# Optimization experiments

Hardware: AMD Instinct MI355X
Metric: run time of the kernel (lower is better)

Reference implementation:

```python
import jax, jax.numpy as jnp
import numpy as np

N_NODES, N_EDGES, N_GRAPHS = 8192, 32768, 256
FXD, HEADS = 78, 10
D2 = FXD * HEADS  # 780
FF = 2048
L_MUT = 735
NF = 32
OUT_DIM = 128


def _ln(x, g, b, eps=1e-5):
    m = x.mean(-1, keepdims=True)
    v = ((x - m) ** 2).mean(-1, keepdims=True)
    return (x - m) * jax.lax.rsqrt(v + eps) * g + b


def _transformer(x, in_w, in_b, out_w, out_b, ln1_g, ln1_b, l1_w, l1_b, l2_w, l2_b, ln2_g, ln2_b):
    # post-LN TransformerEncoderLayer, nhead=1, seq = all N nodes, batch = 1 (eval: dropout off)
    E = x.shape[-1]
    q, k, v = jnp.split(x @ in_w.T + in_b, 3, axis=-1)
    a = jax.nn.softmax((q @ k.T) * (1.0 / np.sqrt(E)), axis=-1) @ v  # [N,N] scores
    x = _ln(x + a @ out_w.T + out_b, ln1_g, ln1_b)
    h = jax.nn.relu(x @ l1_w.T + l1_b) @ l2_w.T + l2_b
    return _ln(x + h, ln2_g, ln2_b)


def _gat(x, src, dst, w, a_src, a_dst, bias):
    # PyG GATConv, heads=10, concat=True, leaky 0.2, self loops already in src/dst
    N = x.shape[0]
    h = (x @ w.T).reshape(N, HEADS, FXD)
    asrc = (h * a_src).sum(-1)  # [N,H]
    adst = (h * a_dst).sum(-1)
    alpha = jax.nn.leaky_relu(asrc[src] + adst[dst], 0.2)  # [E,H]
    amax = jax.lax.stop_gradient(jax.ops.segment_max(alpha, dst, num_segments=N))
    ex = jnp.exp(alpha - amax[dst])
    coef = ex / (jax.ops.segment_sum(ex, dst, num_segments=N)[dst] + 1e-16)
    out = jax.ops.segment_sum(coef[:, :, None] * h[src], dst, num_segments=N)
    return out.reshape(N, HEADS * FXD) + bias


def _gcn(x, src, dst, w, b):
    # PyG GCNConv with self loops (already in src/dst), symmetric norm
    N = x.shape[0]
    deg = jax.ops.segment_sum(jnp.ones(dst.shape, x.dtype), dst, num_segments=N)
    dis = jnp.where(deg > 0, jax.lax.rsqrt(jnp.maximum(deg, 1.0)), 0.0)
    norm = dis[src] * dis[dst]
    return jax.ops.segment_sum(norm[:, None] * (x @ w.T)[src], dst, num_segments=N) + b


def _conv1d(x, w, b):
    y = jax.lax.conv_general_dilated(x, w, (1,), 'VALID', dimension_numbers=('NCH', 'OIH', 'NCH'))
    return y + b[None, :, None]


def _convT1d(x, w, b):
    # torch ConvTranspose1d weight [in,out,k] -> flipped [out,in,k], full padding
    k = w.shape[-1]
    ker = jnp.flip(w, -1).transpose(1, 0, 2)
    y = jax.lax.conv_general_dilated(x, ker, (1,), [(k - 1, k - 1)], dimension_numbers=('NCH', 'OIH', 'NCH'))
    return y + b[None, :, None]


def _maxpool1d(x, k):
    return jax.lax.reduce_window(x, -jnp.inf, jax.lax.max, (1, 1, k), (1, 1, k), 'VALID')


def _bn_eval(x, g, b, eps=1e-5):
    # eval-mode BatchNorm1d with fresh running stats (mean 0, var 1)
    return x * (g / np.sqrt(1.0 + eps))[None, :, None] + b[None, :, None]


def _forward(edge_index, batch, x, target_mut, t1_in_w, t1_in_b, t1_out_w, t1_out_b, t1_ln1_g, t1_ln1_b, t1_l1_w, t1_l1_b, t1_l2_w, t1_l2_b, t1_ln2_g, t1_ln2_b, gat_w, gat_asrc, gat_adst, gat_b, t2_in_w, t2_in_b, t2_out_w, t2_out_b, t2_ln1_g, t2_ln1_b, t2_l1_w, t2_l1_b, t2_l2_w, t2_l2_b, t2_ln2_g, t2_ln2_b, gcn_w, gcn_b, fcg1_w, fcg1_b, fcg2_w, fcg2_b, e1_w, e1_b, bn1_g, bn1_b, e2_w, e2_b, bn2_g, bn2_b, e3_w, e3_b, enc_lin_w, enc_lin_b, d3_w, d3_b, dbn2_g, dbn2_b, d2_w, d2_b, dbn1_g, dbn1_b, d1_w, d1_b, fc1_w, fc1_b, fc2_w, fc2_b, out_w, out_b):
    N = x.shape[0]
    xg = _transformer(x, t1_in_w, t1_in_b, t1_out_w, t1_out_b, t1_ln1_g, t1_ln1_b, t1_l1_w, t1_l1_b, t1_l2_w, t1_l2_b, t1_ln2_g, t1_ln2_b)
    loops = jnp.arange(N, dtype=edge_index.dtype)
    src = jnp.concatenate([edge_index[0], loops])
    dst = jnp.concatenate([edge_index[1], loops])
    xg = jax.nn.relu(_gat(xg, src, dst, gat_w, gat_asrc, gat_adst, gat_b))
    xg = _transformer(xg, t2_in_w, t2_in_b, t2_out_w, t2_out_b, t2_ln1_g, t2_ln1_b, t2_l1_w, t2_l1_b, t2_l2_w, t2_l2_b, t2_ln2_g, t2_ln2_b)
    xg = jax.nn.relu(_gcn(xg, src, dst, gcn_w, gcn_b))
    gm = jax.ops.segment_max(xg, batch, num_segments=N_GRAPHS)
    gm = jnp.where(jnp.isfinite(gm), gm, 0.0)
    cnt = jax.ops.segment_sum(jnp.ones((N,), xg.dtype), batch, num_segments=N_GRAPHS)
    ga = jax.ops.segment_sum(xg, batch, num_segments=N_GRAPHS) / jnp.maximum(cnt, 1.0)[:, None]
    xd = jnp.concatenate([gm, ga], axis=1)  # [B, 1560]
    xd = jax.nn.relu(xd @ fcg1_w.T + fcg1_b)
    xd = xd @ fcg2_w.T + fcg2_b  # [B, 128]
    # conv1d autoencoder on mutation profile
    t = target_mut[:, None, :]  # [B,1,735]
    e = jax.nn.leaky_relu(_bn_eval(_maxpool1d(_conv1d(t, e1_w, e1_b), 8), bn1_g, bn1_b))
    e = jax.nn.leaky_relu(_bn_eval(_maxpool1d(_conv1d(e, e2_w, e2_b), 7), bn2_g, bn2_b))
    e = _conv1d(e, e3_w, e3_b)  # [B,128,5]
    z = e.reshape(e.shape[0], -1) @ enc_lin_w.T + enc_lin_b  # [B,128]
    d = jnp.repeat(jax.nn.leaky_relu(_bn_eval(_convT1d(e, d3_w, d3_b), dbn2_g, dbn2_b)), 7, axis=-1)
    d = jnp.repeat(jax.nn.leaky_relu(_bn_eval(_convT1d(d, d2_w, d2_b), dbn1_g, dbn1_b)), 8, axis=-1)
    decode = _convT1d(d, d1_w, d1_b)  # [B,1,735]
    xc = jnp.concatenate([xd, z], axis=1)
    xc = jax.nn.relu(xc @ fc1_w.T + fc1_b)
    xc = jax.nn.relu(xc @ fc2_w.T + fc2_b)
    out = jax.nn.sigmoid(xc @ out_w.T + out_b)
    return (out, xd, decode)


def setup_inputs():
    key = jax.random.key(0)
    ks = iter(jax.random.split(key, 64))

    def rn(*shape):
        return jax.random.normal(next(ks), shape, jnp.float32) * 0.05

    inp = {}
    inp['x'] = jax.random.normal(next(ks), (N_NODES, FXD), jnp.float32)
    inp['edge_index'] = jax.random.randint(next(ks), (2, N_EDGES), 0, N_NODES)
    inp['batch'] = jnp.sort(jax.random.randint(next(ks), (N_NODES,), 0, N_GRAPHS))
    inp['target_mut'] = jax.random.normal(next(ks), (N_GRAPHS, L_MUT), jnp.float32)
    for p, E in (('t1', FXD), ('t2', D2)):
        inp[p + '_in_w'] = rn(3 * E, E); inp[p + '_in_b'] = jnp.zeros((3 * E,))
        inp[p + '_out_w'] = rn(E, E); inp[p + '_out_b'] = jnp.zeros((E,))
        inp[p + '_ln1_g'] = jnp.ones((E,)); inp[p + '_ln1_b'] = jnp.zeros((E,))
        inp[p + '_l1_w'] = rn(FF, E); inp[p + '_l1_b'] = jnp.zeros((FF,))
        inp[p + '_l2_w'] = rn(E, FF); inp[p + '_l2_b'] = jnp.zeros((E,))
        inp[p + '_ln2_g'] = jnp.ones((E,)); inp[p + '_ln2_b'] = jnp.zeros((E,))
    inp['gat_w'] = rn(D2, FXD); inp['gat_asrc'] = rn(HEADS, FXD); inp['gat_adst'] = rn(HEADS, FXD); inp['gat_b'] = jnp.zeros((D2,))
    inp['gcn_w'] = rn(D2, D2); inp['gcn_b'] = jnp.zeros((D2,))
    inp['fcg1_w'] = rn(1500, 2 * D2); inp['fcg1_b'] = jnp.zeros((1500,))
    inp['fcg2_w'] = rn(OUT_DIM, 1500); inp['fcg2_b'] = jnp.zeros((OUT_DIM,))
    inp['e1_w'] = rn(NF, 1, 8); inp['e1_b'] = jnp.zeros((NF,))
    inp['bn1_g'] = jnp.ones((NF,)); inp['bn1_b'] = jnp.zeros((NF,))
    inp['e2_w'] = rn(2 * NF, NF, 8); inp['e2_b'] = jnp.zeros((2 * NF,))
    inp['bn2_g'] = jnp.ones((2 * NF,)); inp['bn2_b'] = jnp.zeros((2 * NF,))
    inp['e3_w'] = rn(4 * NF, 2 * NF, 8); inp['e3_b'] = jnp.zeros((4 * NF,))
    inp['enc_lin_w'] = rn(OUT_DIM, 640); inp['enc_lin_b'] = jnp.zeros((OUT_DIM,))
    inp['d3_w'] = rn(4 * NF, 2 * NF, 8); inp['d3_b'] = jnp.zeros((2 * NF,))
    inp['dbn2_g'] = jnp.ones((2 * NF,)); inp['dbn2_b'] = jnp.zeros((2 * NF,))
    inp['d2_w'] = rn(2 * NF, NF, 8); inp['d2_b'] = jnp.zeros((NF,))
    inp['dbn1_g'] = jnp.ones((NF,)); inp['dbn1_b'] = jnp.zeros((NF,))
    inp['d1_w'] = rn(NF, 1, 8); inp['d1_b'] = jnp.zeros((1,))
    inp['fc1_w'] = rn(1024, 2 * OUT_DIM); inp['fc1_b'] = jnp.zeros((1024,))
    inp['fc2_w'] = rn(128, 1024); inp['fc2_b'] = jnp.zeros((128,))
    inp['out_w'] = rn(1, 128); inp['out_b'] = jnp.zeros((1,))
    return inp


def reference(x, edge_index, batch, target_mut, t1_in_w, t1_in_b, t1_out_w, t1_out_b, t1_ln1_g, t1_ln1_b, t1_l1_w, t1_l1_b, t1_l2_w, t1_l2_b, t1_ln2_g, t1_ln2_b, gat_w, gat_asrc, gat_adst, gat_b, t2_in_w, t2_in_b, t2_out_w, t2_out_b, t2_ln1_g, t2_ln1_b, t2_l1_w, t2_l1_b, t2_l2_w, t2_l2_b, t2_ln2_g, t2_ln2_b, gcn_w, gcn_b, fcg1_w, fcg1_b, fcg2_w, fcg2_b, e1_w, e1_b, bn1_g, bn1_b, e2_w, e2_b, bn2_g, bn2_b, e3_w, e3_b, enc_lin_w, enc_lin_b, d3_w, d3_b, dbn2_g, dbn2_b, d2_w, d2_b, dbn1_g, dbn1_b, d1_w, d1_b, fc1_w, fc1_b, fc2_w, fc2_b, out_w, out_b):
    return _forward(edge_index, batch, x, target_mut, t1_in_w, t1_in_b, t1_out_w, t1_out_b, t1_ln1_g, t1_ln1_b, t1_l1_w, t1_l1_b, t1_l2_w, t1_l2_b, t1_ln2_g, t1_ln2_b, gat_w, gat_asrc, gat_adst, gat_b, t2_in_w, t2_in_b, t2_out_w, t2_out_b, t2_ln1_g, t2_ln1_b, t2_l1_w, t2_l1_b, t2_l2_w, t2_l2_b, t2_ln2_g, t2_ln2_b, gcn_w, gcn_b, fcg1_w, fcg1_b, fcg2_w, fcg2_b, e1_w, e1_b, bn1_g, bn1_b, e2_w, e2_b, bn2_g, bn2_b, e3_w, e3_b, enc_lin_w, enc_lin_b, d3_w, d3_b, dbn2_g, dbn2_b, d2_w, d2_b, dbn1_g, dbn1_b, d1_w, d1_b, fc1_w, fc1_b, fc2_w, fc2_b, out_w, out_b)
```

## Files before the change

### kernel.cpp

```cpp
#include <hip/hip_runtime.h>
#include <math.h>

#define NN     8192
#define NEDGE  32768
#define NETOT  40960
#define NG     256
#define FXD_   78
#define NH     10
#define DD2    780
#define FFD    2048
#define LMUT   735

static inline int cdiv_i(long long a, int b){ return (int)((a + (long long)b - 1) / b); }
static inline int pad32(int x){ return (x + 31) & ~31; }

typedef __attribute__((ext_vector_type(8))) short bf16x8;
typedef __attribute__((ext_vector_type(4))) float f32x4;

static __device__ __forceinline__ unsigned short f2bf(float f){
    unsigned u = __float_as_uint(f);
    u += 0x7FFFu + ((u >> 16) & 1u);
    return (unsigned short)(u >> 16);
}

static __device__ __forceinline__ void gload16(const void* g, void* l){
    __builtin_amdgcn_global_load_lds((const __attribute__((address_space(1))) void*)g,
                                     (__attribute__((address_space(3))) void*)l, 16, 0, 0);
}

__global__ void fill_f32_k(float* __restrict__ p, float v, long long n){
    long long i = (long long)blockIdx.x * 256 + threadIdx.x;
    if (i < n) p[i] = v;
}
__global__ void fill_u32_k(unsigned* __restrict__ p, unsigned v, long long n){
    long long i = (long long)blockIdx.x * 256 + threadIdx.x;
    if (i < n) p[i] = v;
}

__global__ void cvt_pad_k(const float* __restrict__ src, unsigned short* __restrict__ dst,
                          long long n , int C, int lds_, int ldd)
{
    long long i = (long long)blockIdx.x * 256 + threadIdx.x;
    if (i >= n) return;
    int r = (int)(i / ldd), c = (int)(i % ldd);
    dst[i] = (c < C) ? f2bf(src[(size_t)r * lds_ + c]) : (unsigned short)0;
}

__global__ void norm_cvt_k(const float* __restrict__ A4, unsigned short* __restrict__ XB,
                           int E, int Ep)
{
    long long i = (long long)blockIdx.x * 256 + threadIdx.x;
    if (i >= (long long)NN * Ep) return;
    int r = (int)(i / Ep), c = (int)(i % Ep);
    XB[i] = (c < E) ? f2bf(A4[(size_t)r * Ep + c] / A4[(size_t)r * Ep + E]) : (unsigned short)0;
}

__global__ void tr_bf16_k(const unsigned short* __restrict__ src, unsigned short* __restrict__ dst,
                          int R, int C, int lds_, int ldd)
{
    __shared__ unsigned short t[32][33];
    int cb = blockIdx.x * 32, rb = blockIdx.y * 32;
    int tx = threadIdx.x & 31, ty = threadIdx.x >> 5;
#pragma unroll
    for (int i = 0; i < 4; ++i){
        int r = rb + ty + i * 8, c = cb + tx;
        t[ty + i * 8][tx] = (r < R && c < C) ? src[(size_t)r * lds_ + c] : (unsigned short)0;
    }
    __syncthreads();
#pragma unroll
    for (int i = 0; i < 4; ++i){
        int dr = cb + ty + i * 8, dc = rb + tx;
        if (dr < C && dc < R) dst[(size_t)dr * ldd + dc] = t[tx][ty + i * 8];
    }
}

__global__ void qkv_bias_k(const float* __restrict__ b3, float* __restrict__ out, int E, int Ep)
{
    int idx = blockIdx.x * 256 + threadIdx.x;
    if (idx >= 3 * Ep) return;
    int s = idx / Ep, c = idx % Ep;
    out[idx] = (c < E) ? b3[s * E + c] : 0.f;
}

__global__ void bias_add_k(float* __restrict__ X, const float* __restrict__ b, long long n, int cols)
{
    long long i = (long long)blockIdx.x * 256 + threadIdx.x;
    if (i < n) X[i] += b[i % cols];
}

template<int OUTC, int ACT, int SPLITK, int BROW, int BN>
__global__ __launch_bounds__(256) void mgemm_k(
    const unsigned short* __restrict__ A, const unsigned short* __restrict__ B,
    const float* __restrict__ bias, void* __restrict__ Cv,
    int M, int N, int Kp, int lda, int ldb, int ldc, int swz, float escale)
{
    constexpr int NFJ   = BN / 32;
    constexpr int TILEA = 128 * 32;
    constexpr int TILEB = BN * 32;
    __shared__ unsigned short As[2 * TILEA];
    __shared__ unsigned short Bs[2 * TILEB];
    const int tid = threadIdx.x;
    const int lane = tid & 63, wid = tid >> 6;
    const int r16 = lane & 15, q = lane >> 4;
    const int wr = (wid >> 1) * 64, wc = (wid & 1) * (BN / 2);

    const int gx = gridDim.x, gy = gridDim.y;
    const int nwg = gx * gy;
    int orig = swz ? ((int)blockIdx.x * gy + (int)blockIdx.y)
                   : ((int)blockIdx.y * gx + (int)blockIdx.x);
    int q8 = nwg >> 3, r8 = nwg & 7;
    int xcd = orig & 7, kk8 = orig >> 3;
    int wgid = (xcd < r8 ? xcd * (q8 + 1) : r8 * (q8 + 1) + (xcd - r8) * q8) + kk8;
    int bx, by;
    if (swz){ by = wgid % gy; bx = wgid / gy; }
    else    { bx = wgid % gx; by = wgid / gx; }
    const int row0 = by * 128, col0 = bx * BN;

    int kbeg = 0, kend = Kp;
    if (SPLITK > 1){
        int nt_ = Kp >> 5, cpt = (nt_ + SPLITK - 1) / SPLITK;
        kbeg = (int)blockIdx.z * cpt * 32;
        kend = min(Kp, kbeg + cpt * 32);
    }

    const int c0 = wid * 128 + lane;
    const int r0a = c0 >> 2, k0a = (c0 & 3) << 3;
    const size_t gA0 = (size_t)min(row0 + r0a, M - 1) * lda + k0a;
    const size_t gA1 = (size_t)min(row0 + r0a + 16, M - 1) * lda + k0a;
    unsigned short* lA = As + wid * 1024;
    size_t gB0 = 0, gB1 = 0;
    unsigned short* lB;
    if (BN == 128){
        gB0 = (size_t)min(col0 + r0a, N - 1) * ldb + k0a;
        gB1 = (size_t)min(col0 + r0a + 16, N - 1) * ldb + k0a;
        lB = Bs + wid * 1024;
    } else {
        const int cb = wid * 64 + lane;
        const int rb_ = cb >> 2, kb_ = (cb & 3) << 3;
        gB0 = (size_t)min(col0 + rb_, N - 1) * ldb + kb_;
        lB = Bs + wid * 512;
    }

    f32x4 acc[4][NFJ];
#pragma unroll
    for (int i = 0; i < 4; ++i)
#pragma unroll
        for (int j = 0; j < NFJ; ++j){ f32x4 z = {0.f, 0.f, 0.f, 0.f}; acc[i][j] = z; }

    const int nt = (kend - kbeg) >> 5;
    if (nt > 0){
        gload16(A + gA0 + kbeg, lA);
        gload16(A + gA1 + kbeg, lA + 512);
        gload16(B + gB0 + kbeg, lB);
        if (BN == 128) gload16(B + gB1 + kbeg, lB + 512);
        __syncthreads();
        int cur = 0;
        for (int t = 0; t < nt; ++t){
            const int k0 = kbeg + (t << 5);
            if (t + 1 < nt){
                const int kn = k0 + 32, nb = cur ^ 1;
                gload16(A + gA0 + kn, lA + nb * TILEA);
                gload16(A + gA1 + kn, lA + nb * TILEA + 512);
                gload16(B + gB0 + kn, lB + nb * TILEB);
                if (BN == 128) gload16(B + gB1 + kn, lB + nb * TILEB + 512);
            }
            const unsigned short* Ab = As + cur * TILEA;
            const unsigned short* Bb = Bs + cur * TILEB;
            bf16x8 af[4], bfv[NFJ];
#pragma unroll
            for (int f = 0; f < 4; ++f)
                af[f] = *(const bf16x8*)(Ab + (size_t)(wr + f * 16 + r16) * 32 + (q << 3));
#pragma unroll
            for (int f = 0; f < NFJ; ++f)
                bfv[f] = *(const bf16x8*)(Bb + (size_t)(wc + f * 16 + r16) * 32 + (q << 3));
#pragma unroll
            for (int fi = 0; fi < 4; ++fi)
#pragma unroll
                for (int fj = 0; fj < NFJ; ++fj)
                    acc[fi][fj] = __builtin_amdgcn_mfma_f32_16x16x32_bf16(af[fi], bfv[fj], acc[fi][fj], 0, 0, 0);
            __syncthreads();
            cur ^= 1;
        }
    }

#pragma unroll
    for (int fi = 0; fi < 4; ++fi){
#pragma unroll
        for (int j = 0; j < 4; ++j){
            int r = row0 + wr + fi * 16 + q * 4 + j;
            if (r >= M) continue;
#pragma unroll
            for (int fj = 0; fj < NFJ; ++fj){
                int c = col0 + wc + fj * 16 + r16;
                if (c >= N) continue;
                float v = acc[fi][fj][j];
                if (SPLITK > 1){
                    atomicAdd((float*)Cv + (size_t)r * ldc + c, v);
                } else {
                    if (bias) v += BROW ? bias[r] : bias[c];
                    if (ACT == 1) v = fmaxf(v, 0.f);
                    if (ACT == 2) v = 1.f / (1.f + expf(-v));
                    if (ACT == 3) v = expf(v * escale);
                    if (OUTC == 0) ((float*)Cv)[(size_t)r * ldc + c] = v;
                    else ((unsigned short*)Cv)[(size_t)r * ldc + c] = f2bf(v);
                }
            }
        }
    }
}

template<int OUTC, int ACT, int SPLITK, int BROW, int BN>
static void mgemm(hipStream_t s, const unsigned short* A, const unsigned short* B,
                  const float* bias, void* C, int M, int N, int Kp,
                  int lda, int ldb, int ldc, int swz, float escale = 1.f)
{
    dim3 g(cdiv_i(N, BN), cdiv_i(M, 128), SPLITK);
    mgemm_k<OUTC, ACT, SPLITK, BROW, BN><<<g, 256, 0, s>>>(A, B, bias, C, M, N, Kp, lda, ldb, ldc, swz, escale);
}

__global__ __launch_bounds__(256) void add_ln_k(
    const float* __restrict__ X, const float* __restrict__ Y, const float* __restrict__ ybias,
    const float* __restrict__ g, const float* __restrict__ b,
    float* __restrict__ out, unsigned short* __restrict__ obf, int E, int Ep)
{
    __shared__ float s1[256], s2[256];
    const int tid = threadIdx.x;
    long long base = (long long)blockIdx.x * E;
    float vals[4];
    float sum = 0.f, sq = 0.f;
    int i = 0;
    for (int c = tid; c < Ep; c += 256, ++i){
        float v = 0.f;
        if (c < E){
            v = X[base + c] + Y[base + c];
            if (ybias) v += ybias[c];
            sum += v; sq += v * v;
        }
        vals[i] = v;
    }
    s1[tid] = sum; s2[tid] = sq; __syncthreads();
    for (int s = 128; s; s >>= 1){
        if (tid < s){ s1[tid] += s1[tid + s]; s2[tid] += s2[tid + s]; }
        __syncthreads();
    }
    float mean = s1[0] / (float)E;
    float var = s2[0] / (float)E - mean * mean;
    if (var < 0.f) var = 0.f;
    float inv = 1.f / sqrtf(var + 1e-5f);
    i = 0;
    for (int c = tid; c < Ep; c += 256, ++i){
        if (c < E){
            float o = (vals[i] - mean) * inv * g[c] + b[c];
            out[base + c] = o;
            if (obf) obf[(size_t)blockIdx.x * Ep + c] = f2bf(o);
        } else if (obf) obf[(size_t)blockIdx.x * Ep + c] = 0;
    }
}

static __device__ __forceinline__ unsigned enc_f(float x){
    unsigned u = __float_as_uint(x);
    return (u & 0x80000000u) ? ~u : (u | 0x80000000u);
}
static __device__ __forceinline__ float dec_f(unsigned u){
    return (u & 0x80000000u) ? __uint_as_float(u & 0x7fffffffu) : __uint_as_float(~u);
}
static __device__ __forceinline__ void edge_sd(const int* __restrict__ ei, int e, int& s, int& d){
    if (e < NEDGE){ s = ei[e]; d = ei[NEDGE + e]; }
    else { s = e - NEDGE; d = e - NEDGE; }
}

__global__ void gat_srcdst_k(const float* __restrict__ h, const float* __restrict__ aw_src,
                             const float* __restrict__ aw_dst, float* __restrict__ asrc,
                             float* __restrict__ adst)
{
    int idx = blockIdx.x * 256 + threadIdx.x;
    if (idx >= NN * NH) return;
    int n = idx / NH, hh = idx % NH;
    const float* hp = h + (long long)n * DD2 + hh * FXD_;
    const float* ws = aw_src + hh * FXD_;
    const float* wd = aw_dst + hh * FXD_;
    float s1 = 0.f, s2 = 0.f;
    for (int f = 0; f < FXD_; ++f){ float v = hp[f]; s1 += v * ws[f]; s2 += v * wd[f]; }
    asrc[idx] = s1; adst[idx] = s2;
}

__global__ void gat_alpha_k(const int* __restrict__ ei, const float* __restrict__ asrc,
                            const float* __restrict__ adst, float* __restrict__ alpha,
                            unsigned* __restrict__ amax)
{
    int idx = blockIdx.x * 256 + threadIdx.x;
    if (idx >= NETOT * NH) return;
    int e = idx / NH, hh = idx % NH;
    int s, d; edge_sd(ei, e, s, d);
    float a = asrc[s * NH + hh] + adst[d * NH + hh];
    a = (a > 0.f) ? a : 0.2f * a;
    alpha[idx] = a;
    atomicMax(&amax[d * NH + hh], enc_f(a));
}

__global__ void gat_expsum_k(const int* __restrict__ ei, float* __restrict__ alpha,
                             const unsigned* __restrict__ amax, float* __restrict__ denom)
{
    int idx = blockIdx.x * 256 + threadIdx.x;
    if (idx >= NETOT * NH) return;
    int e = idx / NH, hh = idx % NH;
    int s, d; edge_sd(ei, e, s, d);
    float m = dec_f(amax[d * NH + hh]);
    float ex = expf(alpha[idx] - m);
    alpha[idx] = ex;
    atomicAdd(&denom[d * NH + hh], ex);
}

__global__ void deg_count_k(const int* __restrict__ ei, int* __restrict__ deg)
{
    int e = blockIdx.x * 256 + threadIdx.x;
    if (e >= NETOT) return;
    int s, d; edge_sd(ei, e, s, d);
    atomicAdd(&deg[d], 1);
}

__global__ __launch_bounds__(256) void csr_off_k(const int* __restrict__ deg,
                                                 int* __restrict__ off, int* __restrict__ cur)
{
    __shared__ int pref[257];
    const int tid = threadIdx.x;
    int loc[32];
    int base = tid * 32, sum = 0;
#pragma unroll
    for (int i = 0; i < 32; ++i){ loc[i] = sum; sum += deg[base + i]; }
    __shared__ int part[256];
    part[tid] = sum; __syncthreads();
    if (tid == 0){
        pref[0] = 0;
        for (int i = 0; i < 256; ++i) pref[i + 1] = pref[i] + part[i];
    }
    __syncthreads();
    int p0 = pref[tid];
#pragma unroll
    for (int i = 0; i < 32; ++i){ off[base + i] = p0 + loc[i]; cur[base + i] = p0 + loc[i]; }
    if (tid == 0) off[NN] = pref[256];
}

__global__ void csr_fill_k(const int* __restrict__ ei, int* __restrict__ cur,
                           int* __restrict__ csr_s, int* __restrict__ csr_e)
{
    int e = blockIdx.x * 256 + threadIdx.x;
    if (e >= NETOT) return;
    int s, d; edge_sd(ei, e, s, d);
    int pos = atomicAdd(&cur[d], 1);
    csr_s[pos] = s; csr_e[pos] = e;
}

__global__ __launch_bounds__(256) void gat_gather_k(
    const int* __restrict__ off, const int* __restrict__ csr_s, const int* __restrict__ csr_e,
    const float* __restrict__ ex, const float* __restrict__ denom,
    const float* __restrict__ hfeat, float* __restrict__ out)
{
    const int d = blockIdx.x, tid = threadIdx.x;
    const int beg = off[d], end = off[d + 1];
    for (int f = tid; f < DD2; f += 256){
        int hh = f / FXD_;
        float acc = 0.f;
        for (int p = beg; p < end; ++p)
            acc += ex[csr_e[p] * NH + hh] * hfeat[(size_t)csr_s[p] * DD2 + f];
        out[(size_t)d * DD2 + f] = acc / (denom[d * NH + hh] + 1e-16f);
    }
}

__global__ __launch_bounds__(256) void gcn_gather_k(
    const int* __restrict__ off, const int* __restrict__ csr_s,
    const float* __restrict__ dis, const float* __restrict__ xw, float* __restrict__ out)
{
    const int d = blockIdx.x, tid = threadIdx.x;
    const int beg = off[d], end = off[d + 1];
    const float dd_ = dis[d];
    for (int f = tid; f < DD2; f += 256){
        float acc = 0.f;
        for (int p = beg; p < end; ++p){
            int s = csr_s[p];
            acc += dis[s] * xw[(size_t)s * DD2 + f];
        }
        out[(size_t)d * DD2 + f] = acc * dd_;
    }
}

__global__ void bias_relu_k(float* __restrict__ X, const float* __restrict__ b,
                            unsigned short* __restrict__ obf, int rows, int cols, int ldp)
{
    long long i = (long long)blockIdx.x * 256 + threadIdx.x;
    if (i >= (long long)rows * ldp) return;
    int r = (int)(i / ldp), c = (int)(i % ldp);
    if (c < cols){
        float v = X[(size_t)r * cols + c] + b[c];
        v = v > 0.f ? v : 0.f;
        X[(size_t)r * cols + c] = v;
        if (obf) obf[i] = f2bf(v);
    } else if (obf) obf[i] = 0;
}

__global__ void dis_k(const int* __restrict__ deg, float* __restrict__ dis)
{
    int n = blockIdx.x * 256 + threadIdx.x;
    if (n >= NN) return;
    float d = (float)deg[n];
    dis[n] = (d > 0.f) ? 1.f / sqrtf(fmaxf(d, 1.f)) : 0.f;
}

__global__ void seg_start_k(const int* __restrict__ batch, int* __restrict__ start)
{
    int n = blockIdx.x * 256 + threadIdx.x;
    if (n >= NN) return;
    int b = batch[n];
    int bp = (n == 0) ? -1 : batch[n - 1];
    for (int g = bp + 1; g <= b; ++g) start[g] = n;
    if (n == NN - 1){
        for (int g = b + 1; g <= NG; ++g) start[g] = NN;
    }
}

__global__ __launch_bounds__(256) void pool_seg_k(const float* __restrict__ xg,
                                                  const int* __restrict__ start,
                                                  unsigned short* __restrict__ xdb)
{
    const int g = blockIdx.x, tid = threadIdx.x;
    const int s0 = start[g], s1 = start[g + 1];
    const float inv = 1.f / fmaxf((float)(s1 - s0), 1.f);
    for (int f = tid; f < DD2; f += 256){
        float mx = 0.f, sm = 0.f;
        for (int n = s0; n < s1; ++n){
            float v = xg[(size_t)n * DD2 + f];
            mx = fmaxf(mx, v); sm += v;
        }
        xdb[(size_t)g * 1568 + f] = f2bf(mx);
        xdb[(size_t)g * 1568 + DD2 + f] = f2bf(sm * inv);
    }
    if (tid < 8) xdb[(size_t)g * 1568 + 1560 + tid] = 0;
}

#define BN_SCALE 0.9999950000374996f

__global__ __launch_bounds__(256) void enc1_b(const float* __restrict__ tm, const float* __restrict__ w,
                                              const float* __restrict__ bias, const float* __restrict__ bng,
                                              const float* __restrict__ bnb, float* __restrict__ out)
{
    __shared__ float xs[736];
    __shared__ float ws[256], bs[32], gs[32], b2[32];
    const int g = blockIdx.x, tid = threadIdx.x;
    for (int i = tid; i < 735; i += 256) xs[i] = tm[(size_t)g * LMUT + i];
    ws[tid] = w[tid];
    if (tid < 32){ bs[tid] = bias[tid]; gs[tid] = bng[tid]; b2[tid] = bnb[tid]; }
    __syncthreads();
    for (int idx = tid; idx < 32 * 91; idx += 256){
        int o = idx / 91, t = idx % 91;
        float mx = -3.4e38f;
        for (int p = 0; p < 8; ++p){
            float s = bs[o];
#pragma unroll
            for (int k = 0; k < 8; ++k) s += xs[t * 8 + p + k] * ws[o * 8 + k];
            mx = fmaxf(mx, s);
        }
        float v = mx * gs[o] * BN_SCALE + b2[o];
        out[(size_t)g * 2912 + idx] = v > 0.f ? v : 0.01f * v;
    }
}

__global__ void i2c_enc2_k(const float* __restrict__ in, unsigned short* __restrict__ A){
    int idx = blockIdx.x * 256 + threadIdx.x;
    if (idx >= NG * 84 * 256) return;
    int col = idx & 255, row = idx >> 8;
    int g = row / 84, u = row % 84;
    int i = col >> 3, k = col & 7;
    A[idx] = f2bf(in[(size_t)g * 2912 + i * 91 + u + k]);
}
__global__ void post_enc2_k(const float* __restrict__ G, const float* __restrict__ b,
                            const float* __restrict__ bng, const float* __restrict__ bnb,
                            float* __restrict__ out){
    int idx = blockIdx.x * 256 + threadIdx.x;
    if (idx >= NG * 768) return;
    int t = idx % 12, o = (idx / 12) & 63, g = idx / 768;
    float mx = -3.4e38f;
#pragma unroll
    for (int p = 0; p < 7; ++p) mx = fmaxf(mx, G[(size_t)(g * 84 + t * 7 + p) * 64 + o]);
    float v = (mx + b[o]) * bng[o] * BN_SCALE + bnb[o];
    out[(size_t)g * 768 + o * 12 + t] = v > 0.f ? v : 0.01f * v;
}
__global__ void i2c_enc3_k(const float* __restrict__ in, unsigned short* __restrict__ A){
    int idx = blockIdx.x * 256 + threadIdx.x;
    if (idx >= NG * 5 * 512) return;
    int col = idx & 511, row = idx >> 9;
    int g = row / 5, t = row % 5;
    int i2 = col >> 3, k = col & 7;
    A[idx] = f2bf(in[(size_t)g * 768 + i2 * 12 + t + k]);
}
__global__ void post_enc3_k(const float* __restrict__ G, const float* __restrict__ b,
                            float* __restrict__ e3o, unsigned short* __restrict__ obf){
    int idx = blockIdx.x * 256 + threadIdx.x;
    if (idx >= NG * 640) return;
    int t = idx % 5, o = (idx / 5) & 127, g = idx / 640;
    float v = G[(size_t)(g * 5 + t) * 128 + o] + b[o];
    e3o[(size_t)g * 640 + o * 5 + t] = v;
    obf[(size_t)g * 640 + o * 5 + t] = f2bf(v);
}
__global__ void wshuf_k(const float* __restrict__ src, unsigned short* __restrict__ dst, int I, int O){
    int idx = blockIdx.x * 256 + threadIdx.x;
    if (idx >= I * O * 8) return;
    int o = idx / (I * 8), rem = idx % (I * 8);
    int i = rem >> 3, j = rem & 7;
    dst[idx] = f2bf(src[(size_t)(i * O + o) * 8 + j]);
}
__global__ void i2c_dec3_k(const float* __restrict__ e3o, unsigned short* __restrict__ A){
    int idx = blockIdx.x * 256 + threadIdx.x;
    if (idx >= NG * 12 * 1024) return;
    int col = idx & 1023, row = idx >> 10;
    int g = row / 12, t = row % 12;
    int i2 = col >> 3, j = col & 7;
    int tt = t - j;
    A[idx] = (tt >= 0 && tt < 5) ? f2bf(e3o[(size_t)g * 640 + i2 * 5 + tt]) : (unsigned short)0;
}
__global__ void post_dec3_k(const float* __restrict__ G, const float* __restrict__ b,
                            const float* __restrict__ bng, const float* __restrict__ bnb,
                            float* __restrict__ dd3){
    int idx = blockIdx.x * 256 + threadIdx.x;
    if (idx >= NG * 768) return;
    int t = idx % 12, o = (idx / 12) & 63, g = idx / 768;
    float v = (G[(size_t)(g * 12 + t) * 64 + o] + b[o]) * bng[o] * BN_SCALE + bnb[o];
    dd3[(size_t)g * 768 + o * 12 + t] = v > 0.f ? v : 0.01f * v;
}
__global__ void i2c_dec2_k(const float* __restrict__ dd3, unsigned short* __restrict__ A){
    int idx = blockIdx.x * 256 + threadIdx.x;
    if (idx >= NG * 91 * 512) return;
    int col = idx & 511, row = idx >> 9;
    int g = row / 91, t = row % 91;
    int i2 = col >> 3, j = col & 7;
    int tt = t - j;
    A[idx] = (tt >= 0 && tt < 84) ? f2bf(dd3[(size_t)g * 768 + i2 * 12 + tt / 7]) : (unsigned short)0;
}
__global__ void post_dec2_k(const float* __restrict__ G, const float* __restrict__ b,
                            const float* __restrict__ bng, const float* __restrict__ bnb,
                            float* __restrict__ dd2){
    int idx = blockIdx.x * 256 + threadIdx.x;
    if (idx >= NG * 2912) return;
    int t = idx % 91, o = (idx / 91) & 31, g = idx / 2912;
    float v = (G[(size_t)(g * 91 + t) * 32 + o] + b[o]) * bng[o] * BN_SCALE + bnb[o];
    dd2[(size_t)g * 2912 + o * 91 + t] = v > 0.f ? v : 0.01f * v;
}

__global__ __launch_bounds__(256) void dec1_b(const float* __restrict__ dd2, const float* __restrict__ w,
                                              const float* __restrict__ bias, float* __restrict__ out)
{
    __shared__ float d2s[32][91];
    __shared__ float ws[256];
    const int g = blockIdx.x, tid = threadIdx.x;
    const int t0 = (int)blockIdx.y * 245;
    for (int i = tid; i < 32 * 91; i += 256) d2s[i / 91][i % 91] = dd2[(size_t)g * 2912 + i];
    ws[tid] = w[tid];
    __syncthreads();
    if (tid < 245){
        int t = t0 + tid;
        int id8[8]; bool ok[8];
#pragma unroll
        for (int j = 0; j < 8; ++j){
            int tt = t - j;
            ok[j] = (tt >= 0 && tt < 728);
            id8[j] = ok[j] ? (tt >> 3) : 0;
        }
        float s = bias[0];
        for (int i2 = 0; i2 < 32; ++i2){
            const float* wp = ws + i2 * 8;
            float a = 0.f;
#pragma unroll
            for (int j = 0; j < 8; ++j) if (ok[j]) a += d2s[i2][id8[j]] * wp[j];
            s += a;
        }
        out[(size_t)g * 735 + t] = s;
    }
}

__global__ void concat_xc_k(const float* __restrict__ xd, const float* __restrict__ z,
                            unsigned short* __restrict__ xcb)
{
    int idx = blockIdx.x * 256 + threadIdx.x;
    if (idx >= NG * 256) return;
    int g = idx >> 8, c = idx & 255;
    xcb[idx] = f2bf((c < 128) ? xd[g * 128 + c] : z[g * 128 + (c - 128)]);
}

extern "C" void kernel_launch(void* const* d_in, const int* in_sizes, int n_in,
                              void* d_out, int out_size, void* d_ws, size_t ws_size,
                              hipStream_t stream)
{
    (void)in_sizes; (void)n_in; (void)out_size;

    const float* x      = (const float*)d_in[0];
    const int*   ei     = (const int*)  d_in[1];
    const int*   batch  = (const int*)  d_in[2];
    const float* tmut   = (const float*)d_in[3];
    const float* t1w[12]; for (int i = 0; i < 12; ++i) t1w[i] = (const float*)d_in[4 + i];
    const float* t2w[12]; for (int i = 0; i < 12; ++i) t2w[i] = (const float*)d_in[16 + i];
    const float* gat_w    = (const float*)d_in[28];
    const float* gat_asrc = (const float*)d_in[29];
    const float* gat_adst = (const float*)d_in[30];
    const float* gat_b    = (const float*)d_in[31];
    const float* gcn_w  = (const float*)d_in[32];
    const float* gcn_b  = (const float*)d_in[33];
    const float* fcg1_w = (const float*)d_in[34];
    const float* fcg1_b = (const float*)d_in[35];
    const float* fcg2_w = (const float*)d_in[36];
    const float* fcg2_b = (const float*)d_in[37];
    const float* e1_w = (const float*)d_in[38]; const float* e1_b = (const float*)d_in[39];
    const float* bn1_g = (const float*)d_in[40]; const float* bn1_b = (const float*)d_in[41];
    const float* e2_w = (const float*)d_in[42]; const float* e2_b = (const float*)d_in[43];
    const float* bn2_g = (const float*)d_in[44]; const float* bn2_b = (const float*)d_in[45];
    const float* e3_w = (const float*)d_in[46]; const float* e3_b = (const float*)d_in[47];
    const float* enc_w = (const float*)d_in[48]; const float* enc_b = (const float*)d_in[49];
    const float* d3_w = (const float*)d_in[50]; const float* d3_b = (const float*)d_in[51];
    const float* dbn2_g = (const float*)d_in[52]; const float* dbn2_b = (const float*)d_in[53];
    const float* d2_w = (const float*)d_in[54]; const float* d2_b = (const float*)d_in[55];
    const float* dbn1_g = (const float*)d_in[56]; const float* dbn1_b = (const float*)d_in[57];
    const float* d1_w = (const float*)d_in[58]; const float* d1_b = (const float*)d_in[59];
    const float* fc1_w = (const float*)d_in[60]; const float* fc1_b = (const float*)d_in[61];
    const float* fc2_w = (const float*)d_in[62]; const float* fc2_b = (const float*)d_in[63];
    const float* outw = (const float*)d_in[64]; const float* outb = (const float*)d_in[65];

    float *A1, *A2, *A3, *A4, *X1f, *QBIASf;
    unsigned short *XB, *QKVb, *Vt, *HbPb;
    unsigned short *WQKVb, *WOUTb, *WL1b, *WL2b, *WGb, *WGCNb, *WFCG1b, *WFCG2b,
                   *WENCb, *WFC1b, *WFC2b, *WOUTWb, *XD16, *FG1b, *E3b, *XCb, *FH1b, *FH2b, *Wcvb;
    float *asrc, *adst, *alpha, *denom, *dis, *c1p, *c2p, *e3o, *zz, *dd3, *dd2b;
    unsigned *amax; int *deg, *seg, *csr_off, *csr_cur, *csr_s, *csr_e;

    auto carve = [&](long long RB) -> size_t {
        char* wp_ = (char*)d_ws;
        auto alc = [&](size_t bytes) -> char* {
            char* p = wp_;
            wp_ += (bytes + 255) & ~(size_t)255;
            return p;
        };
        A1 = (float*)alc((size_t)NN * DD2 * 4);
        A2 = (float*)alc((size_t)NN * DD2 * 4);
        A3 = (float*)alc((size_t)NN * DD2 * 4);
        A4 = (float*)alc((size_t)NN * 800 * 4);
        X1f = (float*)alc((size_t)NN * FXD_ * 4);
        XB   = (unsigned short*)alc((size_t)NN * 800 * 2);
        QKVb = (unsigned short*)alc((size_t)NN * 2400 * 2);
        Vt   = (unsigned short*)alc((size_t)801 * NN * 2);
        size_t hb = (size_t)NN * FFD * 2, pb = (size_t)RB * NN * 2;
        HbPb = (unsigned short*)alc(hb > pb ? hb : pb);
        WQKVb = (unsigned short*)alc((size_t)2400 * 800 * 2);
        QBIASf= (float*)alc((size_t)2400 * 4);
        WOUTb = (unsigned short*)alc((size_t)780 * 800 * 2);
        WL1b  = (unsigned short*)alc((size_t)2048 * 800 * 2);
        WL2b  = (unsigned short*)alc((size_t)780 * 2048 * 2);
        WGb   = (unsigned short*)alc((size_t)780 * 96 * 2);
        WGCNb = (unsigned short*)alc((size_t)780 * 800 * 2);
        WFCG1b= (unsigned short*)alc((size_t)1500 * 1568 * 2);
        WFCG2b= (unsigned short*)alc((size_t)128 * 1504 * 2);
        WENCb = (unsigned short*)alc((size_t)128 * 640 * 2);
        WFC1b = (unsigned short*)alc((size_t)1024 * 256 * 2);
        WFC2b = (unsigned short*)alc((size_t)128 * 1024 * 2);
        WOUTWb= (unsigned short*)alc((size_t)128 * 2);
        Wcvb  = (unsigned short*)alc((size_t)128 * 1024 * 2);
        XD16  = (unsigned short*)alc((size_t)NG * 1568 * 2);
        FG1b  = (unsigned short*)alc((size_t)NG * 1504 * 2);
        E3b   = (unsigned short*)alc((size_t)NG * 640 * 2);
        XCb   = (unsigned short*)alc((size_t)NG * 256 * 2);
        FH1b  = (unsigned short*)alc((size_t)NG * 1024 * 2);
        FH2b  = (unsigned short*)alc((size_t)NG * 128 * 2);
        asrc = (float*)alc((size_t)NN * NH * 4);
        adst = (float*)alc((size_t)NN * NH * 4);
        alpha= (float*)alc((size_t)NETOT * NH * 4);
        amax = (unsigned*)alc((size_t)NN * NH * 4);
        denom= (float*)alc((size_t)NN * NH * 4);
        deg  = (int*)alc((size_t)NN * 4);
        dis  = (float*)alc((size_t)NN * 4);
        seg  = (int*)alc((size_t)(NG + 1) * 4);
        csr_off = (int*)alc((size_t)(NN + 1) * 4);
        csr_cur = (int*)alc((size_t)NN * 4);
        csr_s   = (int*)alc((size_t)NETOT * 4);
        csr_e   = (int*)alc((size_t)NETOT * 4);
        c1p  = (float*)alc((size_t)NG * 32 * 91 * 4);
        c2p  = (float*)alc((size_t)NG * 64 * 12 * 4);
        e3o  = (float*)alc((size_t)NG * 128 * 5 * 4);
        zz   = (float*)alc((size_t)NG * 128 * 4);
        dd3  = (float*)alc((size_t)NG * 64 * 12 * 4);
        dd2b = (float*)alc((size_t)NG * 32 * 91 * 4);
        return (size_t)(wp_ - (char*)d_ws);
    };

    long long RB = 512;
    const long long cands[3] = {2048, 1024, 512};
    for (int i = 0; i < 3; ++i){ if (carve(cands[i]) <= ws_size){ RB = cands[i]; break; } }
    carve(RB);
    unsigned short* Pb = HbPb;
    unsigned short* AIM = HbPb;

    float* out0   = (float*)d_out;
    float* xd_out = (float*)d_out + NG;
    float* decode = (float*)d_out + NG + NG * 128;

    auto cvt = [&](const float* src, unsigned short* dst, int R, int C, int lds_, int ldd){
        long long n = (long long)R * ldd;
        cvt_pad_k<<<cdiv_i(n, 256), 256, 0, stream>>>(src, dst, n, C, lds_, ldd);
    };
    auto zero16 = [&](unsigned short* p, long long nshorts){
        fill_u32_k<<<cdiv_i(nshorts / 2, 256), 256, 0, stream>>>((unsigned*)p, 0u, nshorts / 2);
    };
    auto zerof = [&](float* p, long long n){
        fill_f32_k<<<cdiv_i(n, 256), 256, 0, stream>>>(p, 0.f, n);
    };

    auto run_tf = [&](const float* xin, const float* const* W, float* outp, int E){
        const int Ep = pad32(E), E3p = 3 * Ep;
        float scale = (float)(1.0 / sqrt((double)E));
        zero16(WQKVb, (long long)E3p * Ep);
        for (int s = 0; s < 3; ++s)
            cvt(W[0] + (size_t)s * E * E, WQKVb + (size_t)s * Ep * Ep, E, E, E, Ep);
        qkv_bias_k<<<cdiv_i(E3p, 256), 256, 0, stream>>>(W[1], QBIASf, E, Ep);
        mgemm<1,0,1,0,128>(stream, XB, WQKVb, QBIASf, QKVb, NN, E3p, Ep, Ep, Ep, E3p, 0);
        {
            dim3 g(cdiv_i(E, 32), cdiv_i(NN, 32));
            tr_bf16_k<<<g, 256, 0, stream>>>(QKVb + 2 * Ep, Vt, NN, E, E3p, NN);
            fill_u32_k<<<cdiv_i(NN / 2, 256), 256, 0, stream>>>((unsigned*)(Vt + (size_t)E * NN),
                                                                0x3F803F80u, NN / 2);
        }
        zerof(A4, (long long)NN * Ep);
        for (long long r0 = 0; r0 < NN; r0 += RB){
            mgemm<1,3,1,0,128>(stream, QKVb + (size_t)r0 * E3p, QKVb + Ep, nullptr, Pb,
                               (int)RB, NN, Ep, E3p, E3p, NN, 1, scale);
            if (E == FXD_)
                mgemm<0,0,8,0,64>(stream, Pb, Vt, nullptr, A4 + (size_t)r0 * Ep,
                                  (int)RB, E + 1, NN, NN, NN, Ep, 0);
            else
                mgemm<0,0,4,0,64>(stream, Pb, Vt, nullptr, A4 + (size_t)r0 * Ep,
                                  (int)RB, E + 1, NN, NN, NN, Ep, 0);
        }
        norm_cvt_k<<<cdiv_i((long long)NN * Ep, 256), 256, 0, stream>>>(A4, XB, E, Ep);
        cvt(W[2], WOUTb, E, E, E, Ep);
        mgemm<0,0,1,0,64>(stream, XB, WOUTb, W[3], A2, NN, E, Ep, Ep, Ep, E, 0);
        add_ln_k<<<NN, 256, 0, stream>>>(xin, A2, nullptr, W[4], W[5], A3, XB, E, Ep);
        cvt(W[6], WL1b, FFD, E, E, Ep);
        mgemm<1,1,1,0,128>(stream, XB, WL1b, W[7], HbPb, NN, FFD, Ep, Ep, Ep, FFD, 0);
        cvt(W[8], WL2b, E, FFD, FFD, FFD);
        mgemm<0,0,1,0,64>(stream, HbPb, WL2b, W[9], A2, NN, E, FFD, FFD, FFD, E, 0);
        add_ln_k<<<NN, 256, 0, stream>>>(A3, A2, nullptr, W[10], W[11], outp, XB, E, Ep);
    };

    cvt(x, XB, NN, FXD_, FXD_, 96);
    run_tf(x, t1w, X1f, FXD_);

    fill_u32_k<<<cdiv_i(NN, 256), 256, 0, stream>>>((unsigned*)deg, 0u, NN);
    deg_count_k<<<cdiv_i(NETOT, 256), 256, 0, stream>>>(ei, deg);
    csr_off_k<<<1, 256, 0, stream>>>(deg, csr_off, csr_cur);
    csr_fill_k<<<cdiv_i(NETOT, 256), 256, 0, stream>>>(ei, csr_cur, csr_s, csr_e);
    seg_start_k<<<cdiv_i(NN, 256), 256, 0, stream>>>(batch, seg);

    cvt(gat_w, WGb, DD2, FXD_, FXD_, 96);
    mgemm<0,0,1,0,64>(stream, XB, WGb, nullptr, A2, NN, DD2, 96, 96, 96, DD2, 0);
    gat_srcdst_k<<<cdiv_i((long long)NN * NH, 256), 256, 0, stream>>>(A2, gat_asrc, gat_adst, asrc, adst);
    fill_u32_k<<<cdiv_i((long long)NN * NH, 256), 256, 0, stream>>>(amax, 0x007FFFFFu, (long long)NN * NH);
    zerof(denom, (long long)NN * NH);
    gat_alpha_k<<<cdiv_i((long long)NETOT * NH, 256), 256, 0, stream>>>(ei, asrc, adst, alpha, amax);
    gat_expsum_k<<<cdiv_i((long long)NETOT * NH, 256), 256, 0, stream>>>(ei, alpha, amax, denom);
    gat_gather_k<<<NN, 256, 0, stream>>>(csr_off, csr_s, csr_e, alpha, denom, A2, A1);
    bias_relu_k<<<cdiv_i((long long)NN * 800, 256), 256, 0, stream>>>(A1, gat_b, XB, NN, DD2, 800);

    run_tf(A1, t2w, A1, DD2);

    dis_k<<<cdiv_i(NN, 256), 256, 0, stream>>>(deg, dis);
    cvt(gcn_w, WGCNb, DD2, DD2, DD2, 800);
    mgemm<0,0,1,0,64>(stream, XB, WGCNb, nullptr, A2, NN, DD2, 800, 800, 800, DD2, 0);
    gcn_gather_k<<<NN, 256, 0, stream>>>(csr_off, csr_s, dis, A2, A3);
    bias_relu_k<<<cdiv_i((long long)NN * DD2, 256), 256, 0, stream>>>(A3, gcn_b, nullptr, NN, DD2, DD2);

    pool_seg_k<<<NG, 256, 0, stream>>>(A3, seg, XD16);
    cvt(fcg1_w, WFCG1b, 1500, 1560, 1560, 1568);
    zerof(A2, (long long)NG * 1500);
    mgemm<0,0,8,0,64>(stream, XD16, WFCG1b, nullptr, A2, NG, 1500, 1568, 1568, 1568, 1500, 0);
    bias_relu_k<<<cdiv_i((long long)NG * 1504, 256), 256, 0, stream>>>(A2, fcg1_b, FG1b, NG, 1500, 1504);
    cvt(fcg2_w, WFCG2b, 128, 1500, 1500, 1504);
    zerof(xd_out, (long long)NG * 128);
    mgemm<0,0,16,0,128>(stream, FG1b, WFCG2b, nullptr, xd_out, NG, 128, 1504, 1504, 1504, 128, 0);
    bias_add_k<<<cdiv_i((long long)NG * 128, 256), 256, 0, stream>>>(xd_out, fcg2_b, (long long)NG * 128, 128);

    enc1_b<<<NG, 256, 0, stream>>>(tmut, e1_w, e1_b, bn1_g, bn1_b, c1p);
    i2c_enc2_k<<<cdiv_i((long long)NG * 84 * 256, 256), 256, 0, stream>>>(c1p, AIM);
    cvt(e2_w, Wcvb, 64, 256, 256, 256);
    mgemm<0,0,1,0,64>(stream, AIM, Wcvb, nullptr, A2, NG * 84, 64, 256, 256, 256, 64, 0);
    post_enc2_k<<<cdiv_i((long long)NG * 768, 256), 256, 0, stream>>>(A2, e2_b, bn2_g, bn2_b, c2p);
    i2c_enc3_k<<<cdiv_i((long long)NG * 5 * 512, 256), 256, 0, stream>>>(c2p, AIM);
    cvt(e3_w, Wcvb, 128, 512, 512, 512);
    zerof(A2, (long long)NG * 5 * 128);
    mgemm<0,0,4,0,128>(stream, AIM, Wcvb, nullptr, A2, NG * 5, 128, 512, 512, 512, 128, 0);
    post_enc3_k<<<cdiv_i((long long)NG * 640, 256), 256, 0, stream>>>(A2, e3_b, e3o, E3b);
    cvt(enc_w, WENCb, 128, 640, 640, 640);
    mgemm<0,0,1,0,128>(stream, E3b, WENCb, enc_b, zz, NG, 128, 640, 640, 640, 128, 0);

    wshuf_k<<<cdiv_i(128 * 64 * 8, 256), 256, 0, stream>>>(d3_w, Wcvb, 128, 64);
    i2c_dec3_k<<<cdiv_i((long long)NG * 12 * 1024, 256), 256, 0, stream>>>(e3o, AIM);
    zerof(A2, (long long)NG * 12 * 64);
    mgemm<0,0,4,0,64>(stream, AIM, Wcvb, nullptr, A2, NG * 12, 64, 1024, 1024, 1024, 64, 0);
    post_dec3_k<<<cdiv_i((long long)NG * 768, 256), 256, 0, stream>>>(A2, d3_b, dbn2_g, dbn2_b, dd3);
    wshuf_k<<<cdiv_i(64 * 32 * 8, 256), 256, 0, stream>>>(d2_w, Wcvb, 64, 32);
    i2c_dec2_k<<<cdiv_i((long long)NG * 91 * 512, 256), 256, 0, stream>>>(dd3, AIM);
    mgemm<0,0,1,0,64>(stream, AIM, Wcvb, nullptr, A2, NG * 91, 32, 512, 512, 512, 32, 0);
    post_dec2_k<<<cdiv_i((long long)NG * 2912, 256), 256, 0, stream>>>(A2, d2_b, dbn1_g, dbn1_b, dd2b);
    { dim3 g(NG, 3); dec1_b<<<g, 256, 0, stream>>>(dd2b, d1_w, d1_b, decode); }

    concat_xc_k<<<cdiv_i((long long)NG * 256, 256), 256, 0, stream>>>(xd_out, zz, XCb);
    cvt(fc1_w, WFC1b, 1024, 256, 256, 256);
    mgemm<1,1,1,0,128>(stream, XCb, WFC1b, fc1_b, FH1b, NG, 1024, 256, 256, 256, 1024, 0);
    cvt(fc2_w, WFC2b, 128, 1024, 1024, 1024);
    zerof(A3, (long long)NG * 128);
    mgemm<0,0,8,0,128>(stream, FH1b, WFC2b, nullptr, A3, NG, 128, 1024, 1024, 1024, 128, 0);
    bias_relu_k<<<cdiv_i((long long)NG * 128, 256), 256, 0, stream>>>(A3, fc2_b, FH2b, NG, 128, 128);
    cvt(outw, WOUTWb, 1, 128, 128, 128);
    mgemm<0,2,1,0,64>(stream, FH2b, WOUTWb, outb, out0, NG, 1, 128, 128, 128, 1, 0);
}
```

Measured before the change: 1.643 ms.

## Fuse first transformer's attention into a flash-style kernel with split-K atomics

For the E=78 transformer, the separate score GEMM (exp epilogue writing the bf16 P matrix) and P·V split-K GEMM are replaced by one fused kernel. Each block takes 128 query rows and a 1024-key chunk, computes exp(QK^T·scale) into LDS, multiplies by V^T (with a ones row for the denominator), and atomically adds partial sums into A4. This removes the round trip of the large NxN score matrix through global memory and the extra launches. It relies on the same no-max-subtraction exp as before and adds fp32 atomic contention across the 8 key chunks.

```diff
diff --git a/kernel.cpp b/kernel.cpp
--- a/kernel.cpp
+++ b/kernel.cpp
@@ -216,6 +216,116 @@
 {
     dim3 g(cdiv_i(N, BN), cdiv_i(M, 128), SPLITK);
     mgemm_k<OUTC, ACT, SPLITK, BROW, BN><<<g, 256, 0, s>>>(A, B, bias, C, M, N, Kp, lda, ldb, ldc, swz, escale);
+}
+
+#define E3P1 288
+__global__ __launch_bounds__(256) void flash_t1_k(
+    const unsigned short* __restrict__ QKV,
+    const unsigned short* __restrict__ Vt,
+    float* __restrict__ A4, float scale)
+{
+    __shared__ unsigned short Ps[128 * 128];
+    __shared__ unsigned short KV[128 * 96];
+    const int tid = threadIdx.x, lane = tid & 63, wid = tid >> 6;
+    const int r16 = lane & 15, q = lane >> 4;
+    const int wr = (wid >> 1) * 64;
+    const int sc = (wid & 1) * 64;
+    const int oc = (wid & 1) * 48;
+    const int qb = (int)blockIdx.x * 128;
+    const int kb = (int)blockIdx.y * 1024;
+
+    bf16x8 qa[4][3];
+#pragma unroll
+    for (int mi = 0; mi < 4; ++mi)
+#pragma unroll
+        for (int kc = 0; kc < 3; ++kc)
+            qa[mi][kc] = *(const bf16x8*)(QKV + (size_t)(qb + wr + mi * 16 + r16) * E3P1 + kc * 32 + (q << 3));
+
+    f32x4 acco[4][3];
+#pragma unroll
+    for (int i = 0; i < 4; ++i)
+#pragma unroll
+        for (int j = 0; j < 3; ++j){ f32x4 z = {0.f, 0.f, 0.f, 0.f}; acco[i][j] = z; }
+
+    for (int t = 0; t < 8; ++t){
+        const int k0 = kb + t * 128;
+#pragma unroll
+        for (int i = 0; i < 6; ++i){
+            int id = tid + i * 256;
+            int row = id / 12, co = (id % 12) << 3;
+            *(bf16x8*)(&KV[row * 96 + co]) =
+                *(const bf16x8*)(QKV + (size_t)(k0 + row) * E3P1 + 96 + co);
+        }
+        __syncthreads();
+        f32x4 accs[4][4];
+#pragma unroll
+        for (int i = 0; i < 4; ++i)
+#pragma unroll
+            for (int j = 0; j < 4; ++j){ f32x4 z = {0.f, 0.f, 0.f, 0.f}; accs[i][j] = z; }
+#pragma unroll
+        for (int kc = 0; kc < 3; ++kc){
+            bf16x8 bk[4];
+#pragma unroll
+            for (int nj = 0; nj < 4; ++nj)
+                bk[nj] = *(const bf16x8*)(&KV[(sc + nj * 16 + r16) * 96 + kc * 32 + (q << 3)]);
+#pragma unroll
+            for (int mi = 0; mi < 4; ++mi)
+#pragma unroll
+                for (int nj = 0; nj < 4; ++nj)
+                    accs[mi][nj] = __builtin_amdgcn_mfma_f32_16x16x32_bf16(qa[mi][kc], bk[nj], accs[mi][nj], 0, 0, 0);
+        }
+        __syncthreads();
+#pragma unroll
+        for (int mi = 0; mi < 4; ++mi)
+#pragma unroll
+            for (int nj = 0; nj < 4; ++nj)
+#pragma unroll
+                for (int j = 0; j < 4; ++j){
+                    int row = wr + mi * 16 + q * 4 + j;
+                    int col = sc + nj * 16 + r16;
+                    Ps[row * 128 + (col ^ ((row & 7) << 3))] = f2bf(expf(accs[mi][nj][j] * scale));
+                }
+#pragma unroll
+        for (int i = 0; i < 6; ++i){
+            int id = tid + i * 256;
+            int row = id / 16, co = (id % 16) << 3;
+            *(bf16x8*)(&KV[row * 128 + (co ^ ((row & 7) << 3))]) =
+                *(const bf16x8*)(Vt + (size_t)row * NN + k0 + co);
+        }
+        __syncthreads();
+#pragma unroll
+        for (int ko = 0; ko < 4; ++ko){
+            bf16x8 pa[4], vb[3];
+#pragma unroll
+            for (int mi = 0; mi < 4; ++mi){
+                int row = wr + mi * 16 + r16;
+                pa[mi] = *(const bf16x8*)(&Ps[row * 128 + ((ko * 32 + (q << 3)) ^ ((row & 7) << 3))]);
+            }
+#pragma unroll
+            for (int nj = 0; nj < 3; ++nj){
+                int row = oc + nj * 16 + r16;
+                vb[nj] = *(const bf16x8*)(&KV[row * 128 + ((ko * 32 + (q << 3)) ^ ((row & 7) << 3))]);
+            }
+#pragma unroll
+            for (int mi = 0; mi < 4; ++mi)
+#pragma unroll
+                for (int nj = 0; nj < 3; ++nj)
+                    acco[mi][nj] = __builtin_amdgcn_mfma_f32_16x16x32_bf16(pa[mi], vb[nj], acco[mi][nj], 0, 0, 0);
+        }
+        __syncthreads();
+    }
+#pragma unroll
+    for (int mi = 0; mi < 4; ++mi)
+#pragma unroll
+        for (int j = 0; j < 4; ++j){
+            int r = qb + wr + mi * 16 + q * 4 + j;
+#pragma unroll
+            for (int nj = 0; nj < 3; ++nj){
+                int c = oc + nj * 16 + r16;
+                if (c <= FXD_)
+                    atomicAdd(A4 + (size_t)r * 96 + c, acco[mi][nj][j]);
+            }
+        }
 }
 
 __global__ __launch_bounds__(256) void add_ln_k(
@@ -724,15 +834,16 @@
                                                                 0x3F803F80u, NN / 2);
         }
         zerof(A4, (long long)NN * Ep);
-        for (long long r0 = 0; r0 < NN; r0 += RB){
-            mgemm<1,3,1,0,128>(stream, QKVb + (size_t)r0 * E3p, QKVb + Ep, nullptr, Pb,
-                               (int)RB, NN, Ep, E3p, E3p, NN, 1, scale);
-            if (E == FXD_)
-                mgemm<0,0,8,0,64>(stream, Pb, Vt, nullptr, A4 + (size_t)r0 * Ep,
-                                  (int)RB, E + 1, NN, NN, NN, Ep, 0);
-            else
+        if (E == FXD_){
+            dim3 g(NN / 128, 8);
+            flash_t1_k<<<g, 256, 0, stream>>>(QKVb, Vt, A4, scale);
+        } else {
+            for (long long r0 = 0; r0 < NN; r0 += RB){
+                mgemm<1,3,1,0,128>(stream, QKVb + (size_t)r0 * E3p, QKVb + Ep, nullptr, Pb,
+                                   (int)RB, NN, Ep, E3p, E3p, NN, 1, scale);
                 mgemm<0,0,4,0,64>(stream, Pb, Vt, nullptr, A4 + (size_t)r0 * Ep,
                                   (int)RB, E + 1, NN, NN, NN, Ep, 0);
+            }
         }
         norm_cvt_k<<<cdiv_i((long long)NN * Ep, 256), 256, 0, stream>>>(A4, XB, E, Ep);
         cvt(W[2], WOUTb, E, E, E, Ep);
```

Result: faster. 1.579 ms (-3.9%).
